# Performance work log

Hardware: AMD Instinct MI355X
Metric: run time of the kernel (lower is better)

The kernel has to match this reference:

```python
import jax, jax.numpy as jnp
import numpy as np

DIM = 3072
NUM_HEADS = 24
HEAD_DIM = DIM // NUM_HEADS        # 128
B = 1
F, H, W = 4, 24, 24
S = F * H * W                      # 2304
EPS = 1e-6
MAX_POS = 1024
C2 = HEAD_DIM // 2                 # 64 rotary channel-pairs per head
CF = C2 - 2 * (C2 // 3)            # 22 pairs for frame axis
CH = C2 // 3                       # 21 pairs each for H and W axes


def rmsnorm(x, g, eps=EPS):
    # fp32 RMSNorm over last dim with affine weight g [DIM]
    xf = x.astype(jnp.float32)
    ms = jnp.mean(xf * xf, axis=-1, keepdims=True)
    return (xf * jax.lax.rsqrt(ms + eps) * g).astype(x.dtype)


def apply_default_rope(x, grid_sizes, freqs):
    # x: [B, S, N, D]; freqs: [1024, C2] angle table; grid_sizes: [B,3] (F,H,W)
    b, s, n, d = x.shape
    gh = grid_sizes[0, 1]
    gw = grid_sizes[0, 2]
    pos = jnp.arange(s)
    fi = pos // (gh * gw)
    hi = (pos % (gh * gw)) // gw
    wi = pos % gw
    # per-position angles, split across (F, H, W) channel groups -> [S, C2]
    theta = jnp.concatenate([
        freqs[fi, :CF],
        freqs[hi, CF:CF + CH],
        freqs[wi, CF + CH:],
    ], axis=-1)
    cos = jnp.cos(theta)[None, :, None, :]
    sin = jnp.sin(theta)[None, :, None, :]
    xp = x.astype(jnp.float32).reshape(b, s, n, d // 2, 2)
    xr, xi = xp[..., 0], xp[..., 1]
    out = jnp.stack([xr * cos - xi * sin, xr * sin + xi * cos], axis=-1)
    return out.reshape(b, s, n, d).astype(x.dtype)


def setup_inputs() -> dict:
    key = jax.random.key(0)
    ks = jax.random.split(key, 10)
    def w(k):
        return jax.random.normal(k, (DIM, DIM), dtype=jnp.float32) * 0.02
    inv = 10000.0 ** (-jnp.arange(C2, dtype=jnp.float32) / C2)
    freqs = jnp.arange(MAX_POS, dtype=jnp.float32)[:, None] * inv[None, :]
    return {
        "x": jax.random.normal(ks[0], (B, S, DIM), dtype=jnp.float32),
        "seq_lens": jnp.full((B,), S, dtype=jnp.int32),
        "grid_sizes": jnp.tile(jnp.array([[F, H, W]], dtype=jnp.int32), (B, 1)),
        "freqs": freqs,
        "wq": w(ks[1]), "bq": jnp.zeros((DIM,), jnp.float32),
        "wk": w(ks[2]), "bk": jnp.zeros((DIM,), jnp.float32),
        "wv": w(ks[3]), "bv": jnp.zeros((DIM,), jnp.float32),
        "wo": w(ks[4]), "bo": jnp.zeros((DIM,), jnp.float32),
        "gq": jnp.ones((DIM,), jnp.float32),
        "gk": jnp.ones((DIM,), jnp.float32),
    }


def reference(x, seq_lens, grid_sizes, freqs, wq, bq, wk, bk, wv, bv, wo, bo, gq, gk):
    b, s = x.shape[:2]
    n, d = NUM_HEADS, HEAD_DIM
    # QKV projections (torch Linear: x @ W.T + b) + fp32 RMSNorm on q, k
    q = rmsnorm(x @ wq.T + bq, gq).reshape(b, s, n, d)
    k = rmsnorm(x @ wk.T + bk, gk).reshape(b, s, n, d)
    v = (x @ wv.T + bv).reshape(b, s, n, d)
    # 3-axis (F,H,W) RoPE on q, k
    q = apply_default_rope(q, grid_sizes, freqs)
    k = apply_default_rope(k, grid_sizes, freqs)
    # non-causal attention with k_lens masking
    scores = jnp.einsum('bqnd,bknd->bnqk', q, k) * (d ** -0.5)
    kmask = jnp.arange(s)[None, :] < seq_lens[:, None]          # [B, S]
    scores = jnp.where(kmask[:, None, None, :], scores, -1e9)
    probs = jax.nn.softmax(scores, axis=-1)
    out = jnp.einsum('bnqk,bknd->bqnd', probs, v).reshape(b, s, n * d)
    return out @ wo.T + bo
```

## Files before the change

### kernel.cpp

```cpp
#include <hip/hip_runtime.h>
#include <hip/hip_bf16.h>
#include <cstdint>

#define S_LEN 2304
#define NDIM  3072
#define NH    24
#define HD    128

typedef unsigned short u16;
typedef __bf16  bf16x8  __attribute__((ext_vector_type(8)));
typedef float   floatx4 __attribute__((ext_vector_type(4)));

__device__ __forceinline__ u16 f2bf(float x) {
  union { __bf16 b; u16 u; } c;
  c.b = (__bf16)x;
  return c.u;
}

__device__ __forceinline__ void async_load16(const void* g, void* l) {
  auto gp = (const __attribute__((address_space(1))) unsigned int*)(unsigned long long)(g);
  auto lp = (__attribute__((address_space(3))) unsigned int*)(unsigned int)(unsigned long long)(l);
  __builtin_amdgcn_global_load_lds(gp, lp, 16, 0, 0);
}

__global__ __launch_bounds__(256) void cvt_all(const float* __restrict__ x,
                                               const float* __restrict__ w0,
                                               const float* __restrict__ w1,
                                               const float* __restrict__ w2,
                                               const float* __restrict__ w3,
                                               u16* __restrict__ xo,
                                               u16* __restrict__ o0,
                                               u16* __restrict__ o1,
                                               u16* __restrict__ o2,
                                               u16* __restrict__ o3) {
  long b = blockIdx.x;
  const float* in; u16* out;
  if (b < 3456) { in = x; out = xo; }
  else {
    long wi = (b - 3456) / 4608;
    b = (b - 3456) % 4608;
    in  = (wi == 0) ? w0 : (wi == 1) ? w1 : (wi == 2) ? w2 : w3;
    out = (wi == 0) ? o0 : (wi == 1) ? o1 : (wi == 2) ? o2 : o3;
  }
  const long f4 = b * 512 + threadIdx.x;
  const float4* in4 = (const float4*)in;
  float4 a = in4[f4];
  float4 c = in4[f4 + 256];
  union { u16 h[4]; uint2 u; } r0, r1;
  r0.h[0] = f2bf(a.x); r0.h[1] = f2bf(a.y); r0.h[2] = f2bf(a.z); r0.h[3] = f2bf(a.w);
  r1.h[0] = f2bf(c.x); r1.h[1] = f2bf(c.y); r1.h[2] = f2bf(c.z); r1.h[3] = f2bf(c.w);
  *(uint2*)(out + f4 * 4)         = r0.u;
  *(uint2*)(out + (f4 + 256) * 4) = r1.u;
}

__device__ __forceinline__ void gemm_core128(const u16* __restrict__ A,
                                             const u16* __restrict__ B,
                                             int bm, int bn,
                                             u16* As, u16* Bs,
                                             floatx4 acc[4][4]) {
  constexpr int K = NDIM;
  const int t = threadIdx.x;
  const int l = t & 63, w = t >> 6;
  const int l15 = l & 15, quad = l >> 4;
  const int wm = (w >> 1) * 64, wn = (w & 1) * 64;

#pragma unroll
  for (int i = 0; i < 4; ++i)
#pragma unroll
    for (int j = 0; j < 4; ++j) acc[i][j] = {0.f, 0.f, 0.f, 0.f};

  for (int kt = 0; kt < K / 64; ++kt) {
    const int k0 = kt * 64;
#pragma unroll
    for (int i = 0; i < 4; ++i) {
      int p = i * 256 + t;
      int r = p >> 3;
      int c = (p & 7) ^ (r & 7);
      async_load16(A + (long)(bm + r) * K + k0 + c * 8, As + p * 8);
      async_load16(B + (long)(bn + r) * K + k0 + c * 8, Bs + p * 8);
    }
    __syncthreads();
#pragma unroll
    for (int kk = 0; kk < 2; ++kk) {
      bf16x8 af[4], bfr[4];
#pragma unroll
      for (int i = 0; i < 4; ++i) {
        int row = wm + i * 16 + l15;
        int cc = kk * 4 + quad;
        af[i] = *(const bf16x8*)(As + (row * 8 + (cc ^ (row & 7))) * 8);
      }
#pragma unroll
      for (int j = 0; j < 4; ++j) {
        int row = wn + j * 16 + l15;
        int cc = kk * 4 + quad;
        bfr[j] = *(const bf16x8*)(Bs + (row * 8 + (cc ^ (row & 7))) * 8);
      }
#pragma unroll
      for (int i = 0; i < 4; ++i)
#pragma unroll
        for (int j = 0; j < 4; ++j)
          acc[i][j] = __builtin_amdgcn_mfma_f32_16x16x32_bf16(af[i], bfr[j], acc[i][j], 0, 0, 0);
    }
    __syncthreads();
  }
}

__global__ __launch_bounds__(256, 2) void gemm_qkv(const u16* __restrict__ A,
                                                   const u16* __restrict__ wq,
                                                   const u16* __restrict__ wk,
                                                   const u16* __restrict__ wv,
                                                   const float* __restrict__ bq,
                                                   const float* __restrict__ bk,
                                                   const float* __restrict__ bv,
                                                   float* __restrict__ qf,
                                                   float* __restrict__ kf,
                                                   u16* __restrict__ vt) {
  __shared__ u16 As[128 * 64];
  __shared__ u16 Bs[128 * 64];
  const int sel = blockIdx.x / 24;
  const int bn = (blockIdx.x % 24) * 128;
  const int bm = blockIdx.y * 128;
  const u16* Bw = (sel == 0) ? wq : (sel == 1) ? wk : wv;
  const float* bias = (sel == 0) ? bq : (sel == 1) ? bk : bv;

  floatx4 acc[4][4];
  gemm_core128(A, Bw, bm, bn, As, Bs, acc);

  const int t = threadIdx.x;
  const int l = t & 63, w = t >> 6;
  const int l15 = l & 15, quad = l >> 4;
  const int wm = (w >> 1) * 64, wn = (w & 1) * 64;

  if (sel < 2) {
    float* C = sel ? kf : qf;
#pragma unroll
    for (int i = 0; i < 4; ++i) {
      const int gm = bm + wm + i * 16 + quad * 4;
#pragma unroll
      for (int j = 0; j < 4; ++j) {
        const int gn = bn + wn + j * 16 + l15;
        const float bb = bias[gn];
#pragma unroll
        for (int r = 0; r < 4; ++r)
          C[(long)(gm + r) * NDIM + gn] = acc[i][j][r] + bb;
      }
    }
  } else {
#pragma unroll
    for (int i = 0; i < 4; ++i) {
      const int gm = bm + wm + i * 16 + quad * 4;
#pragma unroll
      for (int j = 0; j < 4; ++j) {
        const int gn = bn + wn + j * 16 + l15;
        const float bb = bias[gn];
        union { u16 h[4]; uint2 u; } o;
#pragma unroll
        for (int r = 0; r < 4; ++r) o.h[r] = f2bf(acc[i][j][r] + bb);
        *(uint2*)(vt + (long)gn * S_LEN + gm) = o.u;
      }
    }
  }
}

__global__ __launch_bounds__(256, 2) void gemm_bt(const u16* __restrict__ A,
                                                  const u16* __restrict__ Bw,
                                                  const float* __restrict__ bias,
                                                  float* __restrict__ C) {
  __shared__ u16 As[128 * 64];
  __shared__ u16 Bs[128 * 64];
  const int bm = blockIdx.y * 128;
  const int bn = blockIdx.x * 128;

  floatx4 acc[4][4];
  gemm_core128(A, Bw, bm, bn, As, Bs, acc);

  const int t = threadIdx.x;
  const int l = t & 63, w = t >> 6;
  const int l15 = l & 15, quad = l >> 4;
  const int wm = (w >> 1) * 64, wn = (w & 1) * 64;
#pragma unroll
  for (int i = 0; i < 4; ++i) {
    const int gm = bm + wm + i * 16 + quad * 4;
#pragma unroll
    for (int j = 0; j < 4; ++j) {
      const int gn = bn + wn + j * 16 + l15;
      const float bb = bias[gn];
#pragma unroll
      for (int r = 0; r < 4; ++r)
        C[(long)(gm + r) * NDIM + gn] = acc[i][j][r] + bb;
    }
  }
}

__global__ __launch_bounds__(256) void rmsnorm_rope(const float* __restrict__ qxf,
                                                    const float* __restrict__ kxf,
                                                    const float* __restrict__ gqp,
                                                    const float* __restrict__ gkp,
                                                    const float* __restrict__ freqs,
                                                    const int* __restrict__ gsz,
                                                    u16* __restrict__ qop,
                                                    u16* __restrict__ kop) {
  const int tok = blockIdx.x;
  const int tid = threadIdx.x;
  const float* xf = blockIdx.y ? kxf : qxf;
  const float* g  = blockIdx.y ? gkp : gqp;
  u16* outp       = blockIdx.y ? kop : qop;
  const float* row = xf + (long)tok * NDIM;
  float4 v[3];
  float ss = 0.f;
#pragma unroll
  for (int p = 0; p < 3; ++p) {
    v[p] = ((const float4*)row)[p * 256 + tid];
    ss += v[p].x * v[p].x + v[p].y * v[p].y + v[p].z * v[p].z + v[p].w * v[p].w;
  }
#pragma unroll
  for (int m = 1; m < 64; m <<= 1) ss += __shfl_xor(ss, m);
  __shared__ float red[4];
  if ((tid & 63) == 0) red[tid >> 6] = ss;
  __syncthreads();
  ss = red[0] + red[1] + red[2] + red[3];
  const float scale = rsqrtf(ss * (1.0f / NDIM) + 1e-6f);

  const int gh = gsz[1], gw = gsz[2];
  const int hw = gh * gw;
  const int fi = tok / hw;
  const int hi = (tok % hw) / gw;
  const int wi = tok % gw;
#pragma unroll
  for (int p = 0; p < 3; ++p) {
    const int e0 = (p * 256 + tid) * 4;
    const float4 gg = ((const float4*)g)[p * 256 + tid];
    const int hh = e0 >> 7;
    const int d = e0 & 127;
    const int c0 = d >> 1;
    int pos0 = (c0 < 22) ? fi : ((c0 < 43) ? hi : wi);
    int pos1 = (c0 + 1 < 22) ? fi : ((c0 + 1 < 43) ? hi : wi);
    float th0 = freqs[pos0 * 64 + c0];
    float th1 = freqs[pos1 * 64 + c0 + 1];
    float s0, cc0, s1, cc1;
    __sincosf(th0, &s0, &cc0);
    __sincosf(th1, &s1, &cc1);
    float x0 = v[p].x * scale * gg.x;
    float x1 = v[p].y * scale * gg.y;
    float x2 = v[p].z * scale * gg.z;
    float x3 = v[p].w * scale * gg.w;
    union { u16 h[4]; uint2 u; } o;
    o.h[0] = f2bf(x0 * cc0 - x1 * s0);
    o.h[1] = f2bf(x0 * s0 + x1 * cc0);
    o.h[2] = f2bf(x2 * cc1 - x3 * s1);
    o.h[3] = f2bf(x2 * s1 + x3 * cc1);
    *(uint2*)(outp + ((long)hh * S_LEN + tok) * HD + d) = o.u;
  }
}

__global__ __launch_bounds__(512, 2) void attn_kern(const u16* __restrict__ qb,
                                                    const u16* __restrict__ kb,
                                                    const u16* __restrict__ vt,
                                                    const int* __restrict__ seq_lens,
                                                    u16* __restrict__ ob) {
  __shared__ u16 Kb[2][64 * 128];
  __shared__ u16 Vb[2][128 * 64];
  __shared__ u16 Ps[256 * 64];
  const int b = blockIdx.x;
  const int xcd = b & 7;
  const int slot = b >> 3;
  const int h = xcd * 3 + slot / 9;
  const int qt = slot % 9;
  const int t = threadIdx.x;
  const int l = t & 63, w = t >> 6;
  const int l15 = l & 15, quad = l >> 4;
  const int seqlen = seq_lens[0];
  const float SC2 = 0.12753102543f;

  const u16* kbase = kb + (long)h * S_LEN * HD;
  const u16* vbase = vt + (long)h * HD * S_LEN;

  bf16x8 qfrag[2][4];
#pragma unroll
  for (int i = 0; i < 2; ++i) {
    const u16* qrow = qb + ((long)h * S_LEN + qt * 256 + w * 32 + i * 16 + l15) * HD + quad * 8;
#pragma unroll
    for (int kk = 0; kk < 4; ++kk) qfrag[i][kk] = *(const bf16x8*)(qrow + kk * 32);
  }

  bf16x8 ones;
#pragma unroll
  for (int i = 0; i < 8; ++i) ones[i] = (__bf16)1.0f;

  floatx4 oacc[2][8];
  floatx4 lacc[2];
#pragma unroll
  for (int i = 0; i < 2; ++i) {
#pragma unroll
    for (int j = 0; j < 8; ++j) oacc[i][j] = {0.f, 0.f, 0.f, 0.f};
    lacc[i] = {0.f, 0.f, 0.f, 0.f};
  }

  auto stage = [&](int kt, int buf) {
#pragma unroll
    for (int i = 0; i < 2; ++i) {
      int p = i * 512 + t;
      int rk = p >> 4;
      int ck = (p & 15) ^ (rk & 15);
      async_load16(kbase + ((long)(kt * 64 + rk)) * HD + ck * 8, &Kb[buf][p * 8]);
      int dv = p >> 3;
      int cv = (p & 7) ^ (dv & 7);
      async_load16(vbase + (long)dv * S_LEN + kt * 64 + cv * 8, &Vb[buf][p * 8]);
    }
  };

  auto step = [&](int kt, int cur) {
    __syncthreads();
    if (kt + 1 < S_LEN / 64) stage(kt + 1, cur ^ 1);

    floatx4 sacc[2][4];
#pragma unroll
    for (int i = 0; i < 2; ++i)
#pragma unroll
      for (int j = 0; j < 4; ++j) sacc[i][j] = {0.f, 0.f, 0.f, 0.f};
    __builtin_amdgcn_s_setprio(1);
#pragma unroll
    for (int kk = 0; kk < 4; ++kk) {
#pragma unroll
      for (int j = 0; j < 4; ++j) {
        int row = j * 16 + l15;
        int cc = kk * 4 + quad;
        bf16x8 bk = *(const bf16x8*)(&Kb[cur][(row * 16 + (cc ^ (row & 15))) * 8]);
        sacc[0][j] = __builtin_amdgcn_mfma_f32_16x16x32_bf16(qfrag[0][kk], bk, sacc[0][j], 0, 0, 0);
        sacc[1][j] = __builtin_amdgcn_mfma_f32_16x16x32_bf16(qfrag[1][kk], bk, sacc[1][j], 0, 0, 0);
      }
    }
    __builtin_amdgcn_s_setprio(0);

    const bool tail = (kt * 64 + 64 > seqlen);
#pragma unroll
    for (int i = 0; i < 2; ++i)
#pragma unroll
      for (int j = 0; j < 4; ++j)
#pragma unroll
        for (int r = 0; r < 4; ++r) {
          float sv = sacc[i][j][r] * SC2;
          if (tail) {
            int col = kt * 64 + j * 16 + l15;
            if (col >= seqlen) sv = -1e30f;
          }
          sacc[i][j][r] = exp2f(sv);
        }

#pragma unroll
    for (int i = 0; i < 2; ++i)
#pragma unroll
      for (int j = 0; j < 4; ++j)
#pragma unroll
        for (int r = 0; r < 4; ++r) {
          int rq = w * 32 + i * 16 + quad * 4 + r;
          int ct = j * 16 + l15;
          int cc = ct >> 3;
          Ps[(rq * 8 + (cc ^ (rq & 7))) * 8 + (ct & 7)] = f2bf(sacc[i][j][r]);
        }

    __builtin_amdgcn_s_setprio(1);
#pragma unroll
    for (int kl = 0; kl < 2; ++kl) {
      bf16x8 ap[2];
#pragma unroll
      for (int i = 0; i < 2; ++i) {
        int row = w * 32 + i * 16 + l15;
        int cc = kl * 4 + quad;
        ap[i] = *(const bf16x8*)(&Ps[(row * 8 + (cc ^ (row & 7))) * 8]);
      }
      lacc[0] = __builtin_amdgcn_mfma_f32_16x16x32_bf16(ap[0], ones, lacc[0], 0, 0, 0);
      lacc[1] = __builtin_amdgcn_mfma_f32_16x16x32_bf16(ap[1], ones, lacc[1], 0, 0, 0);
#pragma unroll
      for (int j = 0; j < 8; ++j) {
        int d = j * 16 + l15;
        int ccv = kl * 4 + quad;
        bf16x8 bv = *(const bf16x8*)(&Vb[cur][(d * 8 + (ccv ^ (d & 7))) * 8]);
        oacc[0][j] = __builtin_amdgcn_mfma_f32_16x16x32_bf16(ap[0], bv, oacc[0][j], 0, 0, 0);
        oacc[1][j] = __builtin_amdgcn_mfma_f32_16x16x32_bf16(ap[1], bv, oacc[1][j], 0, 0, 0);
      }
    }
    __builtin_amdgcn_s_setprio(0);
  };

  stage(0, 0);
  for (int kt = 0; kt < S_LEN / 64; kt += 2) {
    step(kt, 0);
    step(kt + 1, 1);
  }

#pragma unroll
  for (int i = 0; i < 2; ++i) {
    float inv[4];
#pragma unroll
    for (int r = 0; r < 4; ++r) inv[r] = 1.0f / lacc[i][r];
#pragma unroll
    for (int j = 0; j < 8; ++j) {
      int gt = qt * 256 + w * 32 + i * 16 + quad * 4;
      int gc = h * HD + j * 16 + l15;
#pragma unroll
      for (int r = 0; r < 4; ++r)
        ob[(long)(gt + r) * NDIM + gc] = f2bf(oacc[i][j][r] * inv[r]);
    }
  }
}

extern "C" void kernel_launch(void* const* d_in, const int* in_sizes, int n_in,
                              void* d_out, int out_size, void* d_ws, size_t ws_size,
                              hipStream_t stream) {
  const float* x        = (const float*)d_in[0];
  const int*   seq_lens = (const int*)  d_in[1];
  const int*   gsz      = (const int*)  d_in[2];
  const float* freqs    = (const float*)d_in[3];
  const float* wq       = (const float*)d_in[4];
  const float* bq       = (const float*)d_in[5];
  const float* wk       = (const float*)d_in[6];
  const float* bk       = (const float*)d_in[7];
  const float* wv       = (const float*)d_in[8];
  const float* bv       = (const float*)d_in[9];
  const float* wo       = (const float*)d_in[10];
  const float* bo       = (const float*)d_in[11];
  const float* gq       = (const float*)d_in[12];
  const float* gk       = (const float*)d_in[13];
  float* out = (float*)d_out;

  char* ws = (char*)d_ws;
  const size_t SD2 = (size_t)S_LEN * NDIM * 2;
  const size_t W2  = (size_t)NDIM * NDIM * 2;
  const size_t SD4 = (size_t)S_LEN * NDIM * 4;
  size_t off = 0;
  u16* xb    = (u16*)(ws + off); off += SD2;
  u16* wqb   = (u16*)(ws + off); off += W2;
  u16* wkb   = (u16*)(ws + off); off += W2;
  u16* wvb   = (u16*)(ws + off); off += W2;
  u16* wob   = (u16*)(ws + off); off += W2;
  float* qf  = (float*)(ws + off); off += SD4;
  float* kf  = (float*)(ws + off); off += SD4;
  u16* vtb   = (u16*)(ws + off); off += SD2;
  u16* qbuf  = (u16*)(ws + off); off += SD2;
  u16* kbuf  = (u16*)(ws + off); off += SD2;
  u16* attnb = (u16*)(ws + off); off += SD2;

  cvt_all<<<3456 + 4 * 4608, 256, 0, stream>>>(x, wq, wk, wv, wo,
                                               xb, wqb, wkb, wvb, wob);

  gemm_qkv<<<dim3(72, 18), 256, 0, stream>>>(xb, wqb, wkb, wvb,
                                             bq, bk, bv, qf, kf, vtb);

  rmsnorm_rope<<<dim3(S_LEN, 2), 256, 0, stream>>>(qf, kf, gq, gk, freqs, gsz,
                                                   qbuf, kbuf);

  attn_kern<<<216, 512, 0, stream>>>(qbuf, kbuf, vtb, seq_lens, attnb);

  gemm_bt<<<dim3(24, 18), 256, 0, stream>>>(attnb, wob, bo, out);
}
```

Before: 515.1 us.

## Keep attention probabilities in registers by computing transposed S tiles

The QK^T MFMA operands are swapped so each lane holds scores for one query and four consecutive keys. The exponentiated probabilities can then be packed straight into the B-operand of the PV MFMA, with V read from LDS as the A operand. This removes the Ps shared-memory round trip and its barrier-free write/read traffic, and lets the output be stored as packed 8-byte writes. V fragments now need two 8-byte LDS reads per MFMA instead of one 16-byte read, which may cause bank conflicts.

```diff
diff --git a/kernel.cpp b/kernel.cpp
--- a/kernel.cpp
+++ b/kernel.cpp
@@ -260,7 +260,6 @@
                                                     u16* __restrict__ ob) {
   __shared__ u16 Kb[2][64 * 128];
   __shared__ u16 Vb[2][128 * 64];
-  __shared__ u16 Ps[256 * 64];
   const int b = blockIdx.x;
   const int xcd = b & 7;
   const int slot = b >> 3;
@@ -287,6 +286,14 @@
 #pragma unroll
   for (int i = 0; i < 8; ++i) ones[i] = (__bf16)1.0f;
 
+  const int lb = l15 & 7;
+  const int qh = quad >> 1;
+  const int q1 = (quad & 1) * 4;
+  int vofs[4];
+#pragma unroll
+  for (int c = 0; c < 4; ++c)
+    vofs[c] = ((qh + c * 2) ^ lb) * 8 + q1;
+
   floatx4 oacc[2][8];
   floatx4 lacc[2];
 #pragma unroll
@@ -322,12 +329,12 @@
 #pragma unroll
     for (int kk = 0; kk < 4; ++kk) {
 #pragma unroll
-      for (int j = 0; j < 4; ++j) {
-        int row = j * 16 + l15;
+      for (int ks = 0; ks < 4; ++ks) {
+        int row = ks * 16 + l15;
         int cc = kk * 4 + quad;
         bf16x8 bk = *(const bf16x8*)(&Kb[cur][(row * 16 + (cc ^ (row & 15))) * 8]);
-        sacc[0][j] = __builtin_amdgcn_mfma_f32_16x16x32_bf16(qfrag[0][kk], bk, sacc[0][j], 0, 0, 0);
-        sacc[1][j] = __builtin_amdgcn_mfma_f32_16x16x32_bf16(qfrag[1][kk], bk, sacc[1][j], 0, 0, 0);
+        sacc[0][ks] = __builtin_amdgcn_mfma_f32_16x16x32_bf16(bk, qfrag[0][kk], sacc[0][ks], 0, 0, 0);
+        sacc[1][ks] = __builtin_amdgcn_mfma_f32_16x16x32_bf16(bk, qfrag[1][kk], sacc[1][ks], 0, 0, 0);
       }
     }
     __builtin_amdgcn_s_setprio(0);
@@ -336,48 +343,38 @@
 #pragma unroll
     for (int i = 0; i < 2; ++i)
 #pragma unroll
-      for (int j = 0; j < 4; ++j)
+      for (int ks = 0; ks < 4; ++ks)
 #pragma unroll
         for (int r = 0; r < 4; ++r) {
-          float sv = sacc[i][j][r] * SC2;
+          float sv = sacc[i][ks][r] * SC2;
           if (tail) {
-            int col = kt * 64 + j * 16 + l15;
-            if (col >= seqlen) sv = -1e30f;
+            int tok = kt * 64 + ks * 16 + quad * 4 + r;
+            if (tok >= seqlen) sv = -1e30f;
           }
-          sacc[i][j][r] = exp2f(sv);
+          sacc[i][ks][r] = exp2f(sv);
         }
 
-#pragma unroll
-    for (int i = 0; i < 2; ++i)
-#pragma unroll
-      for (int j = 0; j < 4; ++j)
-#pragma unroll
-        for (int r = 0; r < 4; ++r) {
-          int rq = w * 32 + i * 16 + quad * 4 + r;
-          int ct = j * 16 + l15;
-          int cc = ct >> 3;
-          Ps[(rq * 8 + (cc ^ (rq & 7))) * 8 + (ct & 7)] = f2bf(sacc[i][j][r]);
-        }
-
     __builtin_amdgcn_s_setprio(1);
 #pragma unroll
-    for (int kl = 0; kl < 2; ++kl) {
-      bf16x8 ap[2];
+    for (int f = 0; f < 2; ++f) {
+      bf16x8 pf[2];
 #pragma unroll
       for (int i = 0; i < 2; ++i) {
-        int row = w * 32 + i * 16 + l15;
-        int cc = kl * 4 + quad;
-        ap[i] = *(const bf16x8*)(&Ps[(row * 8 + (cc ^ (row & 7))) * 8]);
-      }
-      lacc[0] = __builtin_amdgcn_mfma_f32_16x16x32_bf16(ap[0], ones, lacc[0], 0, 0, 0);
-      lacc[1] = __builtin_amdgcn_mfma_f32_16x16x32_bf16(ap[1], ones, lacc[1], 0, 0, 0);
-#pragma unroll
-      for (int j = 0; j < 8; ++j) {
-        int d = j * 16 + l15;
-        int ccv = kl * 4 + quad;
-        bf16x8 bv = *(const bf16x8*)(&Vb[cur][(d * 8 + (ccv ^ (d & 7))) * 8]);
-        oacc[0][j] = __builtin_amdgcn_mfma_f32_16x16x32_bf16(ap[0], bv, oacc[0][j], 0, 0, 0);
-        oacc[1][j] = __builtin_amdgcn_mfma_f32_16x16x32_bf16(ap[1], bv, oacc[1][j], 0, 0, 0);
+#pragma unroll
+        for (int j = 0; j < 4; ++j) pf[i][j] = (__bf16)sacc[i][f * 2][j];
+#pragma unroll
+        for (int j = 0; j < 4; ++j) pf[i][4 + j] = (__bf16)sacc[i][f * 2 + 1][j];
+      }
+      lacc[0] = __builtin_amdgcn_mfma_f32_16x16x32_bf16(ones, pf[0], lacc[0], 0, 0, 0);
+      lacc[1] = __builtin_amdgcn_mfma_f32_16x16x32_bf16(ones, pf[1], lacc[1], 0, 0, 0);
+#pragma unroll
+      for (int dblk = 0; dblk < 8; ++dblk) {
+        const int rowb = (dblk * 16 + l15) * 64;
+        union { bf16x8 v; uint2 u2[2]; } vf;
+        vf.u2[0] = *(const uint2*)(&Vb[cur][rowb + vofs[f * 2]]);
+        vf.u2[1] = *(const uint2*)(&Vb[cur][rowb + vofs[f * 2 + 1]]);
+        oacc[0][dblk] = __builtin_amdgcn_mfma_f32_16x16x32_bf16(vf.v, pf[0], oacc[0][dblk], 0, 0, 0);
+        oacc[1][dblk] = __builtin_amdgcn_mfma_f32_16x16x32_bf16(vf.v, pf[1], oacc[1][dblk], 0, 0, 0);
       }
     }
     __builtin_amdgcn_s_setprio(0);
@@ -391,16 +388,14 @@
 
 #pragma unroll
   for (int i = 0; i < 2; ++i) {
-    float inv[4];
-#pragma unroll
-    for (int r = 0; r < 4; ++r) inv[r] = 1.0f / lacc[i][r];
-#pragma unroll
-    for (int j = 0; j < 8; ++j) {
-      int gt = qt * 256 + w * 32 + i * 16 + quad * 4;
-      int gc = h * HD + j * 16 + l15;
-#pragma unroll
-      for (int r = 0; r < 4; ++r)
-        ob[(long)(gt + r) * NDIM + gc] = f2bf(oacc[i][j][r] * inv[r]);
+    const float inv = 1.0f / lacc[i][0];
+    const long gt = qt * 256 + w * 32 + i * 16 + l15;
+#pragma unroll
+    for (int dblk = 0; dblk < 8; ++dblk) {
+      union { u16 h[4]; uint2 u; } o;
+#pragma unroll
+      for (int r = 0; r < 4; ++r) o.h[r] = f2bf(oacc[i][dblk][r] * inv);
+      *(uint2*)(ob + gt * NDIM + h * HD + dblk * 16 + quad * 4) = o.u;
     }
   }
 }
```

Result: no change. 523.7 us (+1.7%).
